# Optimization experiments

Hardware: AMD Instinct MI355X
Metric: run time of the kernel (lower is better)

The kernel has to match this reference:

```python
import jax, jax.numpy as jnp
import numpy as np
import math

N = 2048       # num_nodes (dense graph)
F_IN = 256     # num_in_features
F_OUT = 256    # num_out_features
H = 8          # num_heads
LN_EPS = 1e-5

# NOTE: every e3nn FullyConnectedTensorProduct in this module maps
# (Fx0e) x irreps_sh -> (Kx0e). Only the l=0 spherical-harmonic component can
# couple scalars to scalars, and Y_0 = 1 under normalization='component'.
# Each TP is therefore exactly a linear map with a 1/sqrt(fan_in) path norm,
# and edge_direction does not enter the math at all.


def setup_inputs() -> dict:
    key = jax.random.key(0)
    ks = jax.random.split(key, 12)
    inv = 1.0 / np.sqrt(F_IN)
    return {
        "node_features": jax.random.normal(ks[0], (N, F_IN), jnp.float32),
        "edges_features_distance": jax.random.uniform(ks[1], (N, N), jnp.float32),
        "edges_features_bond": jax.random.uniform(ks[2], (N, N), jnp.float32),
        "edge_direction": jax.random.normal(ks[3], (N * N, 3), jnp.float32),
        "degree_matrix": jax.random.randint(ks[4], (N, N), 0, 2).astype(jnp.float32),
        # tensor-product weights (xavier-ish scale)
        "Wq": jax.random.normal(ks[5], (F_IN, H), jnp.float32) * inv,
        "Wk": jax.random.normal(ks[6], (F_IN, H), jnp.float32) * inv,
        "Wv": jax.random.normal(ks[7], (F_IN, F_OUT), jnp.float32) * inv,
        "w_bond": jax.random.normal(ks[8], (), jnp.float32),
        "w_bond_contrib": jax.random.normal(ks[9], (), jnp.float32),
        "w_gauss": jax.random.normal(ks[10], (), jnp.float32),
    }


def reference(node_features, edges_features_distance, edges_features_bond,
              edge_direction, degree_matrix, Wq, Wk, Wv,
              w_bond, w_bond_contrib, w_gauss):
    scale = 1.0 / jnp.sqrt(jnp.asarray(F_IN, node_features.dtype))
    # scalar-only tensor products == scaled linears (Y_0 = 1)
    q = (node_features @ Wq) * scale              # [N, H]
    k = (node_features @ Wk) * scale              # [N, H]
    v = (node_features @ Wv) * scale              # [N, F_OUT]

    # raw_attention[i,j,h] = (q_i + k_i)/sqrt(H)  (key.transpose(0,1) picks node i)
    qk = (q + k) / math.sqrt(H)                   # [N, H]
    bond = edges_features_bond * (w_bond * w_bond_contrib)   # [N, N]
    gauss = edges_features_distance * w_gauss                 # [N, N]
    raw = qk[:, None, :] + (bond + gauss)[:, :, None]          # [N, N, H]

    mask = jnp.where(degree_matrix > 0, 0.0, -1e9).astype(raw.dtype)
    scores = jax.nn.leaky_relu(raw, 0.2) + mask[:, :, None]
    # torch F.softmax without dim on a 3-D tensor -> dim=0
    attn = jax.nn.softmax(scores, axis=0)          # [N, N, H]
    # F.dropout treated as identity (eval / deterministic baseline)
    attn_mean = attn.mean(axis=2)                  # [N, N]

    # aggregated[i] = sum_j attn_mean[i,j] * v_j  (value[i,j,:] = v(node_j))
    aggregated = attn_mean @ v                     # [N, F_OUT]
    updated_nodes = jax.nn.elu(aggregated)

    # no_grad connectivity update
    un = jax.lax.stop_gradient(updated_nodes)
    sim = un @ un.T                                # [N, N]
    dd = -jax.lax.stop_gradient(edges_features_distance)
    conn = jax.nn.sigmoid(sim) * dd * jax.lax.stop_gradient(degree_matrix)
    mu = conn.mean(axis=-1, keepdims=True)
    var = conn.var(axis=-1, keepdims=True)
    conn = (conn - mu) * jax.lax.rsqrt(var + LN_EPS)
    conn = conn + conn.T
    return updated_nodes, conn
```

## Files before the change

kernel.cpp:

```cpp
#include <hip/hip_runtime.h>
#include <hip/hip_bf16.h>

#define NN 2048
#define FIN 256
#define FOUT 256
#define HH 8

typedef short bhalf8 __attribute__((ext_vector_type(8)));
typedef float f32x4  __attribute__((ext_vector_type(4)));

__device__ __forceinline__ unsigned short f2b(float f) {
    __hip_bfloat16 h = __float2bfloat16(f);
    return *reinterpret_cast<unsigned short*>(&h);
}
__device__ __forceinline__ float b2f(unsigned short u) {
    __hip_bfloat16 h = *reinterpret_cast<__hip_bfloat16*>(&u);
    return __bfloat162float(h);
}

__global__ __launch_bounds__(256) void k1_qkv(
    const float* __restrict__ x, const float* __restrict__ Wq,
    const float* __restrict__ Wk, const float* __restrict__ Wv,
    float* __restrict__ v, float* __restrict__ qk)
{
    const int ib = blockIdx.x * 4;
    const int t  = threadIdx.x;
    __shared__ float xs[4][FIN];
    __shared__ float part[256];
    #pragma unroll
    for (int n = 0; n < 4; ++n) xs[n][t] = x[(long)(ib+n)*FIN + t];
    __syncthreads();
    float a0 = 0.f, a1 = 0.f, a2 = 0.f, a3 = 0.f;
    #pragma unroll 4
    for (int c = 0; c < FIN; ++c) {
        const float wv = Wv[c*FOUT + t];
        a0 = fmaf(xs[0][c], wv, a0); a1 = fmaf(xs[1][c], wv, a1);
        a2 = fmaf(xs[2][c], wv, a2); a3 = fmaf(xs[3][c], wv, a3);
    }
    v[(ib+0)*FOUT + t] = a0 * 0.0625f;
    v[(ib+1)*FOUT + t] = a1 * 0.0625f;
    v[(ib+2)*FOUT + t] = a2 * 0.0625f;
    v[(ib+3)*FOUT + t] = a3 * 0.0625f;
    {
        const int n = t >> 6, h = t & 7, seg = (t >> 3) & 7;
        float a = 0.f;
        for (int c = seg*32; c < seg*32 + 32; ++c)
            a = fmaf(xs[n][c], Wq[c*HH + h] + Wk[c*HH + h], a);
        part[t] = a;
    }
    __syncthreads();
    if (t < 32) {
        const int n = t >> 3, h = t & 7;
        float a = 0.f;
        #pragma unroll
        for (int s2 = 0; s2 < 8; ++s2) a += part[n*64 + s2*8 + h];
        qk[(ib+n)*HH + h] = a * (0.0625f * 0.35355339059327373f);
    }
}

__global__ __launch_bounds__(256) void k1b_vT(
    const float* __restrict__ v, unsigned short* __restrict__ vtb)
{
    const int k0 = blockIdx.x * 64;
    const int f0 = blockIdx.y * 64;
    const int t  = threadIdx.x;
    __shared__ float LT[64][68];
    const int r  = t >> 4;
    const int c4 = (t & 15) * 4;
    #pragma unroll
    for (int p = 0; p < 4; ++p) {
        const float4 q = *(const float4*)&v[(k0 + r + p*16)*FOUT + f0 + c4];
        LT[c4+0][r + p*16] = q.x; LT[c4+1][r + p*16] = q.y;
        LT[c4+2][r + p*16] = q.z; LT[c4+3][r + p*16] = q.w;
    }
    __syncthreads();
    #pragma unroll
    for (int p = 0; p < 4; ++p) {
        const int fr = r + p*16;
        ushort4 ub;
        ub.x = f2b(LT[fr][c4+0]); ub.y = f2b(LT[fr][c4+1]);
        ub.z = f2b(LT[fr][c4+2]); ub.w = f2b(LT[fr][c4+3]);
        *(ushort4*)&vtb[(long)(f0 + fr)*NN + k0 + c4] = ub;
    }
}

__global__ __launch_bounds__(256) void k2_denom(
    const float* __restrict__ bond, const float* __restrict__ dist,
    const float* __restrict__ deg, const float* __restrict__ qk,
    const float* __restrict__ wb, const float* __restrict__ wbc,
    const float* __restrict__ wg, float* __restrict__ D,
    unsigned short* __restrict__ fbuf, unsigned short* __restrict__ ddb)
{
    const float cb = wb[0] * wbc[0];
    const float cg = wg[0];
    const int tx = threadIdx.x & 63, ty = threadIdx.x >> 6;
    const int j  = blockIdx.x * 64 + tx;
    const int i0 = blockIdx.y * 64;
    __shared__ float qs[64*8];
    for (int p = threadIdx.x; p < 64*8; p += 256) qs[p] = qk[i0*8 + p];
    __syncthreads();
    float acc[8];
    #pragma unroll
    for (int h = 0; h < 8; ++h) acc[h] = 0.f;
    for (int ii = ty; ii < 64; ii += 4) {
        const long idx = (long)(i0 + ii)*NN + j;
        const float dv = dist[idx];
        const float gv = deg[idx];
        const float s0 = fmaf(cb, bond[idx], cg * dv);
        const unsigned short fb = f2b((gv > 0.f) ? s0 : -__builtin_inff());
        fbuf[idx] = fb;
        ddb[idx]  = f2b(-dv * gv);
        const float s = b2f(fb);
        #pragma unroll
        for (int h = 0; h < 8; ++h) {
            float r = qs[ii*8 + h] + s;
            r = (r > 0.f) ? r : 0.2f*r;
            acc[h] += __expf(r);
        }
    }
    __shared__ float red[4][64][8];
    #pragma unroll
    for (int h = 0; h < 8; ++h) red[ty][tx][h] = acc[h];
    __syncthreads();
    for (int p = threadIdx.x; p < 512; p += 256) {
        const int jj = p >> 3, h = p & 7;
        const float ssum = red[0][jj][h] + red[1][jj][h] + red[2][jj][h] + red[3][jj][h];
        atomicAdd(&D[(blockIdx.x*64 + jj)*8 + h], ssum);
    }
}

__global__ __launch_bounds__(256) void k3_attnmean(
    const unsigned short* __restrict__ fbuf, const float* __restrict__ qk,
    const float* __restrict__ D, unsigned short* __restrict__ amb)
{
    const int tx = threadIdx.x & 63, ty = threadIdx.x >> 6;
    const int j  = blockIdx.x * 64 + tx;
    const int i0 = blockIdx.y * 64;
    __shared__ float qs[64*8];
    for (int p = threadIdx.x; p < 64*8; p += 256) qs[p] = qk[i0*8 + p];
    __syncthreads();
    float invD[8];
    #pragma unroll
    for (int h = 0; h < 8; ++h) invD[h] = 0.125f / fmaxf(D[j*8 + h], 1e-30f);
    for (int ii = ty; ii < 64; ii += 4) {
        const long idx = (long)(i0 + ii)*NN + j;
        const float s = b2f(fbuf[idx]);
        float o = 0.f;
        #pragma unroll
        for (int h = 0; h < 8; ++h) {
            float r = qs[ii*8 + h] + s;
            r = (r > 0.f) ? r : 0.2f*r;
            o = fmaf(__expf(r), invD[h], o);
        }
        amb[idx] = f2b(o);
    }
}

__global__ __launch_bounds__(256) void k4_aggr(
    const unsigned short* __restrict__ amb,
    const unsigned short* __restrict__ vtb, float* __restrict__ partial)
{
    const int i0 = blockIdx.x * 64;
    const int f0 = blockIdx.y * 64;
    const int k0 = blockIdx.z * 512;
    const int w  = threadIdx.x >> 6;
    const int l  = threadIdx.x & 63;
    const int lm = l & 15, lq = l >> 4;
    const int iw = i0 + w*16;
    f32x4 acc[4] = {f32x4{0,0,0,0}, f32x4{0,0,0,0}, f32x4{0,0,0,0}, f32x4{0,0,0,0}};
    for (int kk = k0; kk < k0 + 512; kk += 32) {
        const bhalf8 a = *(const bhalf8*)&amb[(long)(iw + lm)*NN + kk + lq*8];
        #pragma unroll
        for (int c = 0; c < 4; ++c) {
            const bhalf8 b = *(const bhalf8*)&vtb[(long)(f0 + c*16 + lm)*NN + kk + lq*8];
            acc[c] = __builtin_amdgcn_mfma_f32_16x16x32_bf16(a, b, acc[c], 0, 0, 0);
        }
    }
    float* out = partial + (long)blockIdx.z * NN * FOUT;
    #pragma unroll
    for (int c = 0; c < 4; ++c)
        #pragma unroll
        for (int r = 0; r < 4; ++r)
            out[(iw + lq*4 + r)*FOUT + f0 + c*16 + lm] = acc[c][r];
}

__global__ __launch_bounds__(256) void k4b_elu(
    const float* __restrict__ partial, float* __restrict__ un,
    unsigned short* __restrict__ unb)
{
    const int idx = blockIdx.x*256 + threadIdx.x;
    const float4* p = (const float4*)partial;
    float4 s = p[idx];
    #pragma unroll
    for (int z = 1; z < 4; ++z) {
        const float4 q = p[idx + z*(NN*FOUT/4)];
        s.x += q.x; s.y += q.y; s.z += q.z; s.w += q.w;
    }
    s.x = (s.x > 0.f) ? s.x : (__expf(s.x) - 1.f);
    s.y = (s.y > 0.f) ? s.y : (__expf(s.y) - 1.f);
    s.z = (s.z > 0.f) ? s.z : (__expf(s.z) - 1.f);
    s.w = (s.w > 0.f) ? s.w : (__expf(s.w) - 1.f);
    ((float4*)un)[idx] = s;
    ushort4 ub; ub.x = f2b(s.x); ub.y = f2b(s.y); ub.z = f2b(s.z); ub.w = f2b(s.w);
    *(ushort4*)&unb[(long)idx*4] = ub;
}

__global__ __launch_bounds__(256) void k5_sim(
    const unsigned short* __restrict__ unb, const unsigned short* __restrict__ ddb,
    unsigned short* __restrict__ c0,
    float* __restrict__ rowsum, float* __restrict__ rowsq)
{
    const int i0 = blockIdx.y * 64;
    const int j0 = blockIdx.x * 64;
    const int w  = threadIdx.x >> 6;
    const int l  = threadIdx.x & 63;
    const int lm = l & 15, lq = l >> 4;
    const int iw = i0 + w*16;
    f32x4 acc[4] = {f32x4{0,0,0,0}, f32x4{0,0,0,0}, f32x4{0,0,0,0}, f32x4{0,0,0,0}};
    for (int kk = 0; kk < FOUT; kk += 32) {
        const bhalf8 a = *(const bhalf8*)&unb[(long)(iw + lm)*FOUT + kk + lq*8];
        #pragma unroll
        for (int c = 0; c < 4; ++c) {
            const bhalf8 b = *(const bhalf8*)&unb[(long)(j0 + c*16 + lm)*FOUT + kk + lq*8];
            acc[c] = __builtin_amdgcn_mfma_f32_16x16x32_bf16(a, b, acc[c], 0, 0, 0);
        }
    }
    float srow[4] = {0.f,0.f,0.f,0.f}, qrow[4] = {0.f,0.f,0.f,0.f};
    #pragma unroll
    for (int c = 0; c < 4; ++c) {
        #pragma unroll
        for (int r = 0; r < 4; ++r) {
            const int i = iw + lq*4 + r;
            const int j = j0 + c*16 + lm;
            const long idx = (long)i*NN + j;
            const float sg = 1.f / (1.f + __expf(-acc[c][r]));
            const float val = sg * b2f(ddb[idx]);
            c0[idx] = f2b(val);
            srow[r] += val;
            qrow[r] = fmaf(val, val, qrow[r]);
        }
    }
    #pragma unroll
    for (int r = 0; r < 4; ++r) {
        #pragma unroll
        for (int m = 8; m >= 1; m >>= 1) {
            srow[r] += __shfl_xor(srow[r], m, 64);
            qrow[r] += __shfl_xor(qrow[r], m, 64);
        }
        if (lm == 0) {
            atomicAdd(&rowsum[iw + lq*4 + r], srow[r]);
            atomicAdd(&rowsq[iw + lq*4 + r],  qrow[r]);
        }
    }
}

__global__ void k6_stats(const float* __restrict__ rowsum,
                         const float* __restrict__ rowsq,
                         float* __restrict__ mu, float* __restrict__ rs)
{
    const int i = blockIdx.x*256 + threadIdx.x;
    if (i < NN) {
        const float m = rowsum[i] * (1.f/NN);
        const float var = rowsq[i] * (1.f/NN) - m*m;
        mu[i] = m;
        rs[i] = rsqrtf(var + 1e-5f);
    }
}

__global__ __launch_bounds__(256) void k7_conn(
    const unsigned short* __restrict__ c0, const float* __restrict__ mu,
    const float* __restrict__ rs, float* __restrict__ out1)
{
    const int i0 = blockIdx.y * 64;
    const int j0 = blockIdx.x * 64;
    const int t  = threadIdx.x;
    __shared__ float LT[64][68];
    __shared__ float muj[64], rsj[64];
    const int r  = t >> 4;
    const int c4 = (t & 15) * 4;
    if (t < 64)        muj[t] = mu[j0 + t];
    else if (t < 128)  rsj[t-64] = rs[j0 + t - 64];
    #pragma unroll
    for (int p = 0; p < 4; ++p) {
        const int jl = r + p*16;
        const ushort4 q = *(const ushort4*)&c0[(long)(j0 + jl)*NN + i0 + c4];
        LT[c4+0][jl] = b2f(q.x); LT[c4+1][jl] = b2f(q.y);
        LT[c4+2][jl] = b2f(q.z); LT[c4+3][jl] = b2f(q.w);
    }
    __syncthreads();
    #pragma unroll
    for (int p = 0; p < 4; ++p) {
        const int rr = r + p*16;
        const int i  = i0 + rr;
        const ushort4 xb = *(const ushort4*)&c0[(long)i*NN + j0 + c4];
        const float mi = mu[i], ri = rs[i];
        float4 o;
        o.x = (b2f(xb.x) - mi)*ri + (LT[rr][c4+0] - muj[c4+0])*rsj[c4+0];
        o.y = (b2f(xb.y) - mi)*ri + (LT[rr][c4+1] - muj[c4+1])*rsj[c4+1];
        o.z = (b2f(xb.z) - mi)*ri + (LT[rr][c4+2] - muj[c4+2])*rsj[c4+2];
        o.w = (b2f(xb.w) - mi)*ri + (LT[rr][c4+3] - muj[c4+3])*rsj[c4+3];
        *(float4*)&out1[(long)i*NN + j0 + c4] = o;
    }
}

extern "C" void kernel_launch(void* const* d_in, const int* in_sizes, int n_in,
                              void* d_out, int out_size, void* d_ws, size_t ws_size,
                              hipStream_t stream)
{
    const float* x    = (const float*)d_in[0];
    const float* dist = (const float*)d_in[1];
    const float* bond = (const float*)d_in[2];
    const float* deg  = (const float*)d_in[4];
    const float* Wq   = (const float*)d_in[5];
    const float* Wk   = (const float*)d_in[6];
    const float* Wv   = (const float*)d_in[7];
    const float* wb   = (const float*)d_in[8];
    const float* wbc  = (const float*)d_in[9];
    const float* wg   = (const float*)d_in[10];

    float* out0 = (float*)d_out;
    float* out1 = out0 + (size_t)NN*FOUT;

    char* w = (char*)d_ws;
    unsigned short* fbuf = (unsigned short*)(w);
    unsigned short* c0   = (unsigned short*)(w);
    unsigned short* amb  = (unsigned short*)(w +  8388608);
    unsigned short* ddb  = (unsigned short*)(w + 16777216);
    float* partial = (float*)(w + 25165824);
    float* v       = (float*)(w + 33554432);
    unsigned short* vtb = (unsigned short*)(w + 35651584);
    unsigned short* unb = (unsigned short*)(w + 36700160);
    float* qk      = (float*)(w + 37748736);
    float* D       = (float*)(w + 37814272);
    float* rowsum  = (float*)(w + 37879808);
    float* rowsq   = (float*)(w + 37888000);
    float* mu      = (float*)(w + 37896192);
    float* rs      = (float*)(w + 37904384);

    hipMemsetAsync(D, 0, 65536 + 8192 + 8192, stream);

    k1_qkv<<<NN/4, 256, 0, stream>>>(x, Wq, Wk, Wv, v, qk);
    dim3 g1b(NN/64, FOUT/64);
    k1b_vT<<<g1b, 256, 0, stream>>>(v, vtb);
    dim3 g23(NN/64, NN/64);
    k2_denom<<<g23, 256, 0, stream>>>(bond, dist, deg, qk, wb, wbc, wg, D, fbuf, ddb);
    k3_attnmean<<<g23, 256, 0, stream>>>(fbuf, qk, D, amb);
    dim3 g4(NN/64, FOUT/64, 4);
    k4_aggr<<<g4, 256, 0, stream>>>(amb, vtb, partial);
    k4b_elu<<<NN*FOUT/4/256, 256, 0, stream>>>(partial, out0, unb);
    dim3 g5(NN/64, NN/64);
    k5_sim<<<g5, 256, 0, stream>>>(unb, ddb, c0, rowsum, rowsq);
    k6_stats<<<8, 256, 0, stream>>>(rowsum, rowsq, mu, rs);
    k7_conn<<<g5, 256, 0, stream>>>(c0, mu, rs, out1);
}
```

Measured before the change: 240.2 us.

## Vectorize softmax kernels and fuse split-K aggregation with ELU epilogue

The denominator and attention-mean kernels now have each thread handle four consecutive columns with float4/ushort4 loads and stores, and each wave covers a contiguous 16-row strip. This cuts per-element instruction overhead and widens memory transactions on the N×N streams. The aggregation GEMM drops the 4-way split-K partial buffer and the separate ELU kernel: each block of 128 threads computes a 32×32 tile over the full K and applies ELU plus the bf16 store in its epilogue. That removes a partial-sum round trip through memory and one launch, but gives fewer, longer-running GEMM blocks with less parallelism per tile.

```diff
diff --git a/kernel.cpp b/kernel.cpp
--- a/kernel.cpp
+++ b/kernel.cpp
@@ -93,39 +93,58 @@
 {
     const float cb = wb[0] * wbc[0];
     const float cg = wg[0];
-    const int tx = threadIdx.x & 63, ty = threadIdx.x >> 6;
-    const int j  = blockIdx.x * 64 + tx;
+    const int t  = threadIdx.x;
+    const int tx = t & 63;
+    const int ty = t >> 6;
+    const int j0 = blockIdx.x * 256;
     const int i0 = blockIdx.y * 64;
+    const int j  = j0 + tx*4;
     __shared__ float qs[64*8];
-    for (int p = threadIdx.x; p < 64*8; p += 256) qs[p] = qk[i0*8 + p];
-    __syncthreads();
-    float acc[8];
-    #pragma unroll
-    for (int h = 0; h < 8; ++h) acc[h] = 0.f;
-    for (int ii = ty; ii < 64; ii += 4) {
-        const long idx = (long)(i0 + ii)*NN + j;
-        const float dv = dist[idx];
-        const float gv = deg[idx];
-        const float s0 = fmaf(cb, bond[idx], cg * dv);
-        const unsigned short fb = f2b((gv > 0.f) ? s0 : -__builtin_inff());
-        fbuf[idx] = fb;
-        ddb[idx]  = f2b(-dv * gv);
-        const float s = b2f(fb);
+    __shared__ float red[4][2048];
+    for (int p = t; p < 512; p += 256) qs[p] = qk[i0*8 + p];
+    __syncthreads();
+    float acc[4][8];
+    #pragma unroll
+    for (int jj = 0; jj < 4; ++jj)
+        #pragma unroll
+        for (int h = 0; h < 8; ++h) acc[jj][h] = 0.f;
+    const int ibase = i0 + ty*16;
+    for (int ii = 0; ii < 16; ++ii) {
+        const long idx = (long)(ibase + ii)*NN + j;
+        const float4 dv = *(const float4*)&dist[idx];
+        const float4 bv = *(const float4*)&bond[idx];
+        const float4 gv = *(const float4*)&deg[idx];
+        ushort4 fb, db;
+        fb.x = f2b((gv.x > 0.f) ? fmaf(cb, bv.x, cg*dv.x) : -__builtin_inff());
+        fb.y = f2b((gv.y > 0.f) ? fmaf(cb, bv.y, cg*dv.y) : -__builtin_inff());
+        fb.z = f2b((gv.z > 0.f) ? fmaf(cb, bv.z, cg*dv.z) : -__builtin_inff());
+        fb.w = f2b((gv.w > 0.f) ? fmaf(cb, bv.w, cg*dv.w) : -__builtin_inff());
+        db.x = f2b(-dv.x * gv.x); db.y = f2b(-dv.y * gv.y);
+        db.z = f2b(-dv.z * gv.z); db.w = f2b(-dv.w * gv.w);
+        *(ushort4*)&fbuf[idx] = fb;
+        *(ushort4*)&ddb[idx]  = db;
+        float s[4];
+        s[0] = b2f(fb.x); s[1] = b2f(fb.y); s[2] = b2f(fb.z); s[3] = b2f(fb.w);
+        const float* qrow = &qs[(ty*16 + ii)*8];
         #pragma unroll
         for (int h = 0; h < 8; ++h) {
-            float r = qs[ii*8 + h] + s;
-            r = (r > 0.f) ? r : 0.2f*r;
-            acc[h] += __expf(r);
-        }
-    }
-    __shared__ float red[4][64][8];
-    #pragma unroll
-    for (int h = 0; h < 8; ++h) red[ty][tx][h] = acc[h];
-    __syncthreads();
-    for (int p = threadIdx.x; p < 512; p += 256) {
-        const int jj = p >> 3, h = p & 7;
-        const float ssum = red[0][jj][h] + red[1][jj][h] + red[2][jj][h] + red[3][jj][h];
-        atomicAdd(&D[(blockIdx.x*64 + jj)*8 + h], ssum);
+            const float q = qrow[h];
+            #pragma unroll
+            for (int jj = 0; jj < 4; ++jj) {
+                float r = q + s[jj];
+                r = fmaxf(r, 0.2f*r);
+                acc[jj][h] += __expf(r);
+            }
+        }
+    }
+    #pragma unroll
+    for (int jj = 0; jj < 4; ++jj)
+        #pragma unroll
+        for (int h = 0; h < 8; ++h) red[ty][(tx*4 + jj)*8 + h] = acc[jj][h];
+    __syncthreads();
+    for (int p = t; p < 2048; p += 256) {
+        const float ssum = red[0][p] + red[1][p] + red[2][p] + red[3][p];
+        atomicAdd(&D[j0*8 + p], ssum);
     }
 }
 
@@ -133,76 +152,87 @@
     const unsigned short* __restrict__ fbuf, const float* __restrict__ qk,
     const float* __restrict__ D, unsigned short* __restrict__ amb)
 {
-    const int tx = threadIdx.x & 63, ty = threadIdx.x >> 6;
-    const int j  = blockIdx.x * 64 + tx;
+    const int t  = threadIdx.x;
+    const int tx = t & 63;
+    const int ty = t >> 6;
+    const int j0 = blockIdx.x * 256;
     const int i0 = blockIdx.y * 64;
+    const int j  = j0 + tx*4;
     __shared__ float qs[64*8];
-    for (int p = threadIdx.x; p < 64*8; p += 256) qs[p] = qk[i0*8 + p];
-    __syncthreads();
-    float invD[8];
-    #pragma unroll
-    for (int h = 0; h < 8; ++h) invD[h] = 0.125f / fmaxf(D[j*8 + h], 1e-30f);
-    for (int ii = ty; ii < 64; ii += 4) {
-        const long idx = (long)(i0 + ii)*NN + j;
-        const float s = b2f(fbuf[idx]);
-        float o = 0.f;
+    for (int p = t; p < 512; p += 256) qs[p] = qk[i0*8 + p];
+    __syncthreads();
+    float invD[4][8];
+    #pragma unroll
+    for (int jj = 0; jj < 4; ++jj) {
+        const float4 d0 = *(const float4*)&D[(j + jj)*8 + 0];
+        const float4 d1 = *(const float4*)&D[(j + jj)*8 + 4];
+        invD[jj][0] = 0.125f / fmaxf(d0.x, 1e-30f);
+        invD[jj][1] = 0.125f / fmaxf(d0.y, 1e-30f);
+        invD[jj][2] = 0.125f / fmaxf(d0.z, 1e-30f);
+        invD[jj][3] = 0.125f / fmaxf(d0.w, 1e-30f);
+        invD[jj][4] = 0.125f / fmaxf(d1.x, 1e-30f);
+        invD[jj][5] = 0.125f / fmaxf(d1.y, 1e-30f);
+        invD[jj][6] = 0.125f / fmaxf(d1.z, 1e-30f);
+        invD[jj][7] = 0.125f / fmaxf(d1.w, 1e-30f);
+    }
+    const int ibase = i0 + ty*16;
+    for (int ii = 0; ii < 16; ++ii) {
+        const long idx = (long)(ibase + ii)*NN + j;
+        const ushort4 fb = *(const ushort4*)&fbuf[idx];
+        float s[4];
+        s[0] = b2f(fb.x); s[1] = b2f(fb.y); s[2] = b2f(fb.z); s[3] = b2f(fb.w);
+        float o[4] = {0.f, 0.f, 0.f, 0.f};
+        const float* qrow = &qs[(ty*16 + ii)*8];
         #pragma unroll
         for (int h = 0; h < 8; ++h) {
-            float r = qs[ii*8 + h] + s;
-            r = (r > 0.f) ? r : 0.2f*r;
-            o = fmaf(__expf(r), invD[h], o);
-        }
-        amb[idx] = f2b(o);
-    }
-}
-
-__global__ __launch_bounds__(256) void k4_aggr(
+            const float q = qrow[h];
+            #pragma unroll
+            for (int jj = 0; jj < 4; ++jj) {
+                float r = q + s[jj];
+                r = fmaxf(r, 0.2f*r);
+                o[jj] = fmaf(__expf(r), invD[jj][h], o[jj]);
+            }
+        }
+        ushort4 ob;
+        ob.x = f2b(o[0]); ob.y = f2b(o[1]); ob.z = f2b(o[2]); ob.w = f2b(o[3]);
+        *(ushort4*)&amb[idx] = ob;
+    }
+}
+
+__global__ __launch_bounds__(128) void k4_aggr(
     const unsigned short* __restrict__ amb,
-    const unsigned short* __restrict__ vtb, float* __restrict__ partial)
-{
-    const int i0 = blockIdx.x * 64;
-    const int f0 = blockIdx.y * 64;
-    const int k0 = blockIdx.z * 512;
+    const unsigned short* __restrict__ vtb,
+    float* __restrict__ out0, unsigned short* __restrict__ unb)
+{
+    const int i0 = blockIdx.x * 32;
+    const int f0 = blockIdx.y * 32;
     const int w  = threadIdx.x >> 6;
     const int l  = threadIdx.x & 63;
     const int lm = l & 15, lq = l >> 4;
     const int iw = i0 + w*16;
-    f32x4 acc[4] = {f32x4{0,0,0,0}, f32x4{0,0,0,0}, f32x4{0,0,0,0}, f32x4{0,0,0,0}};
-    for (int kk = k0; kk < k0 + 512; kk += 32) {
-        const bhalf8 a = *(const bhalf8*)&amb[(long)(iw + lm)*NN + kk + lq*8];
-        #pragma unroll
-        for (int c = 0; c < 4; ++c) {
-            const bhalf8 b = *(const bhalf8*)&vtb[(long)(f0 + c*16 + lm)*NN + kk + lq*8];
-            acc[c] = __builtin_amdgcn_mfma_f32_16x16x32_bf16(a, b, acc[c], 0, 0, 0);
-        }
-    }
-    float* out = partial + (long)blockIdx.z * NN * FOUT;
-    #pragma unroll
-    for (int c = 0; c < 4; ++c)
-        #pragma unroll
-        for (int r = 0; r < 4; ++r)
-            out[(iw + lq*4 + r)*FOUT + f0 + c*16 + lm] = acc[c][r];
-}
-
-__global__ __launch_bounds__(256) void k4b_elu(
-    const float* __restrict__ partial, float* __restrict__ un,
-    unsigned short* __restrict__ unb)
-{
-    const int idx = blockIdx.x*256 + threadIdx.x;
-    const float4* p = (const float4*)partial;
-    float4 s = p[idx];
-    #pragma unroll
-    for (int z = 1; z < 4; ++z) {
-        const float4 q = p[idx + z*(NN*FOUT/4)];
-        s.x += q.x; s.y += q.y; s.z += q.z; s.w += q.w;
-    }
-    s.x = (s.x > 0.f) ? s.x : (__expf(s.x) - 1.f);
-    s.y = (s.y > 0.f) ? s.y : (__expf(s.y) - 1.f);
-    s.z = (s.z > 0.f) ? s.z : (__expf(s.z) - 1.f);
-    s.w = (s.w > 0.f) ? s.w : (__expf(s.w) - 1.f);
-    ((float4*)un)[idx] = s;
-    ushort4 ub; ub.x = f2b(s.x); ub.y = f2b(s.y); ub.z = f2b(s.z); ub.w = f2b(s.w);
-    *(ushort4*)&unb[(long)idx*4] = ub;
+    f32x4 acc0 = {0,0,0,0}, acc1 = {0,0,0,0};
+    const unsigned short* arow  = &amb[(long)(iw + lm)*NN + lq*8];
+    const unsigned short* brow0 = &vtb[(long)(f0 + lm)*NN + lq*8];
+    const unsigned short* brow1 = &vtb[(long)(f0 + 16 + lm)*NN + lq*8];
+    #pragma unroll 4
+    for (int kk = 0; kk < NN; kk += 32) {
+        const bhalf8 a  = *(const bhalf8*)&arow[kk];
+        const bhalf8 b0 = *(const bhalf8*)&brow0[kk];
+        const bhalf8 b1 = *(const bhalf8*)&brow1[kk];
+        acc0 = __builtin_amdgcn_mfma_f32_16x16x32_bf16(a, b0, acc0, 0, 0, 0);
+        acc1 = __builtin_amdgcn_mfma_f32_16x16x32_bf16(a, b1, acc1, 0, 0, 0);
+    }
+    #pragma unroll
+    for (int r = 0; r < 4; ++r) {
+        const int i = iw + lq*4 + r;
+        float s0 = acc0[r], s1 = acc1[r];
+        s0 = (s0 > 0.f) ? s0 : (__expf(s0) - 1.f);
+        s1 = (s1 > 0.f) ? s1 : (__expf(s1) - 1.f);
+        out0[(long)i*FOUT + f0 + lm]      = s0;
+        out0[(long)i*FOUT + f0 + 16 + lm] = s1;
+        unb[(long)i*FOUT + f0 + lm]       = f2b(s0);
+        unb[(long)i*FOUT + f0 + 16 + lm]  = f2b(s1);
+    }
 }
 
 __global__ __launch_bounds__(256) void k5_sim(
@@ -326,7 +356,6 @@
     unsigned short* c0   = (unsigned short*)(w);
     unsigned short* amb  = (unsigned short*)(w +  8388608);
     unsigned short* ddb  = (unsigned short*)(w + 16777216);
-    float* partial = (float*)(w + 25165824);
     float* v       = (float*)(w + 33554432);
     unsigned short* vtb = (unsigned short*)(w + 35651584);
     unsigned short* unb = (unsigned short*)(w + 36700160);
@@ -342,12 +371,11 @@
     k1_qkv<<<NN/4, 256, 0, stream>>>(x, Wq, Wk, Wv, v, qk);
     dim3 g1b(NN/64, FOUT/64);
     k1b_vT<<<g1b, 256, 0, stream>>>(v, vtb);
-    dim3 g23(NN/64, NN/64);
+    dim3 g23(NN/256, NN/64);
     k2_denom<<<g23, 256, 0, stream>>>(bond, dist, deg, qk, wb, wbc, wg, D, fbuf, ddb);
     k3_attnmean<<<g23, 256, 0, stream>>>(fbuf, qk, D, amb);
-    dim3 g4(NN/64, FOUT/64, 4);
-    k4_aggr<<<g4, 256, 0, stream>>>(amb, vtb, partial);
-    k4b_elu<<<NN*FOUT/4/256, 256, 0, stream>>>(partial, out0, unb);
+    dim3 g4(NN/32, FOUT/32);
+    k4_aggr<<<g4, 128, 0, stream>>>(amb, vtb, out0, unb);
     dim3 g5(NN/64, NN/64);
     k5_sim<<<g5, 256, 0, stream>>>(unb, ddb, c0, rowsum, rowsq);
     k6_stats<<<8, 256, 0, stream>>>(rowsum, rowsq, mu, rs);
```

Measured after the change: 250.8 us. 4.4% more time.
